# Kernel tuning notes

Hardware: AMD Instinct MI355X
Metric: run time of the kernel (lower is better)

Reference implementation:

```python
import jax, jax.numpy as jnp
import numpy as np

N, K, CIN, C, ET = 16, 128, 64, 64, 2  # batch, nodes, in-dim, hidden, edge types


def setup_inputs() -> dict:
    key = jax.random.key(0)
    ks = jax.random.split(key, 12)
    s = 0.05  # weight init scale
    return {
        "t": jnp.full((1,), 0.5, jnp.float32),
        "x": jax.random.normal(ks[0], (N, K, CIN), jnp.float32),
        "E": jax.random.uniform(ks[1], (N, K, K, ET), jnp.float32),
        # ConcatLinear: Linear(CIN+1 -> C) on cat([t, x])
        "W_lin": jax.random.normal(ks[2], (CIN + 1, C), jnp.float32) * s,
        "b_lin": jnp.zeros((C,), jnp.float32),
        # unary_passing: Linear(C,C) -> tanh -> Linear(C,C)
        "W_u1": jax.random.normal(ks[3], (C, C), jnp.float32) * s,
        "b_u1": jnp.zeros((C,), jnp.float32),
        "W_u2": jax.random.normal(ks[4], (C, C), jnp.float32) * s,
        "b_u2": jnp.zeros((C,), jnp.float32),
        # binary_passing[e]: Linear(2C,C) -> tanh -> Linear(C,C), stacked over edge types
        "W_b1": jax.random.normal(ks[5], (ET, 2 * C, C), jnp.float32) * s,
        "b_b1": jnp.zeros((ET, C), jnp.float32),
        "W_b2": jax.random.normal(ks[6], (ET, C, C), jnp.float32) * s,
        "b_b2": jnp.zeros((ET, C), jnp.float32),
    }


def reference(t, x, E, W_lin, b_lin, W_u1, b_u1, W_u2, b_u2, W_b1, b_b1, W_b2, b_b2):
    n, k, _ = x.shape
    # ConcatLinear: h = Linear(cat([t, x]))  -> [N, K, C]
    tt = jnp.broadcast_to(t.reshape(1, 1, 1).astype(x.dtype), (n, k, 1))
    h = jnp.concatenate([tt, x], axis=-1) @ W_lin + b_lin
    c = h.shape[-1]
    # unary message: MLP over nodes
    unary = jnp.tanh(h @ W_u1 + b_u1) @ W_u2 + b_u2  # [N, K, C]
    # all-pairs tensor: pair[n, i, j] = cat(h[n, j], h[n, i])  -> [N, K, K, 2C]
    pair = jnp.concatenate(
        [
            jnp.broadcast_to(h[:, None, :, :], (n, k, k, c)),
            jnp.broadcast_to(h[:, :, None, :], (n, k, k, c)),
        ],
        axis=-1,
    )
    # per-edge-type MLP (vectorized over edge types)
    hid = jnp.tanh(jnp.einsum('nijd,edh->enijh', pair, W_b1) + b_b1[:, None, None, None, :])
    msg = jnp.einsum('enijh,ehc->enijc', hid, W_b2) + b_b2[:, None, None, None, :]
    # weight by edge matrix and sum over edge types -> [N, K, K, C]
    msg = (msg * jnp.moveaxis(E, -1, 0)[..., None]).sum(axis=0)
    # reduce over sender dim (dim 1) and normalize by K
    binary = msg.sum(axis=1) / k  # [N, K, C]
    return unary + binary
```

## Files before the change

### kernel.cpp

```cpp
#include <hip/hip_runtime.h>

#define NB 16
#define KK 128
#define CC 64

__device__ __forceinline__ float tanh_from_e2x(float e2x) {
    return 1.f - 2.f * __builtin_amdgcn_rcpf(e2x + 1.f);
}

__global__ __launch_bounds__(256) void precompute_kernel(
    const float* __restrict__ t, const float* __restrict__ x,
    const float* __restrict__ W_lin, const float* __restrict__ b_lin,
    const float* __restrict__ W_u1, const float* __restrict__ b_u1,
    const float* __restrict__ W_u2, const float* __restrict__ b_u2,
    const float* __restrict__ W_b1, const float* __restrict__ b_b1,
    float* __restrict__ A2, float* __restrict__ B2, float* __restrict__ unary)
{
    const int tid  = threadIdx.x;
    const int lane = tid & 63;
    const int r    = blockIdx.x * 4 + (tid >> 6);

    const float xv = x[r * CC + lane];
    float h = fmaf(t[0], W_lin[lane], b_lin[lane]);
#pragma unroll 8
    for (int k = 0; k < CC; ++k) {
        float xk = __shfl(xv, k);
        h = fmaf(xk, W_lin[(k + 1) * CC + lane], h);
    }

    float u1 = b_u1[lane];
    float a0 = b_b1[lane], a1 = b_b1[CC + lane];
    float bb0 = 0.f, bb1 = 0.f;
#pragma unroll 4
    for (int k = 0; k < CC; ++k) {
        float hk = __shfl(h, k);
        u1  = fmaf(hk, W_u1[k * CC + lane], u1);
        a0  = fmaf(hk, W_b1[k * CC + lane], a0);
        bb0 = fmaf(hk, W_b1[(CC + k) * CC + lane], bb0);
        a1  = fmaf(hk, W_b1[2 * CC * CC + k * CC + lane], a1);
        bb1 = fmaf(hk, W_b1[2 * CC * CC + (CC + k) * CC + lane], bb1);
    }

    float tu = tanh_from_e2x(__expf(2.f * u1));
    float u2 = b_u2[lane];
#pragma unroll 8
    for (int k = 0; k < CC; ++k) {
        float uk = __shfl(tu, k);
        u2 = fmaf(uk, W_u2[k * CC + lane], u2);
    }

    const int idx = r * CC + lane;
    unary[idx] = u2;
    ((float2*)A2)[idx] = make_float2(2.f * a0, 2.f * a1);
    ((float2*)B2)[idx] = make_float2(2.f * bb0, 2.f * bb1);
}

__global__ __launch_bounds__(256) void binary_kernel(
    const float* __restrict__ E, const float* __restrict__ W_b2,
    const float* __restrict__ b_b2, const float* __restrict__ A2,
    const float* __restrict__ B2, const float* __restrict__ unary,
    float* __restrict__ out)
{
    __shared__ float Bs[KK * CC * 2];
    __shared__ float Es[4 * KK * 2];
    __shared__ float Gs[4 * CC * 2];

    const int tid = threadIdx.x;
    const int bid = blockIdx.x;
    const int n   = bid >> 5;
    const int j0  = (bid & 31) * 4;

    const float4* Bsrc = (const float4*)(B2 + n * KK * CC * 2);
    float4* Bdst = (float4*)Bs;
#pragma unroll
    for (int it = 0; it < 16; ++it) Bdst[tid + it * 256] = Bsrc[tid + it * 256];

    const float2* E2 = (const float2*)E;
    float2* Es2 = (float2*)Es;
#pragma unroll
    for (int it = 0; it < 2; ++it) {
        int v = tid + it * 256;
        int wv = v >> 7, i = v & 127;
        Es2[wv * KK + i] = E2[(n * KK + i) * KK + (j0 + wv)];
    }
    __syncthreads();

    const int lane = tid & 63;
    const int w    = tid >> 6;
    const int r    = n * KK + j0 + w;

    const float2 a2 = ((const float2*)A2)[r * CC + lane];
    const float2* BsRow = (const float2*)Bs;
    const float2* EsW   = ((const float2*)Es) + w * KK;

    float G0 = 0.f, G1 = 0.f;
#pragma unroll 8
    for (int i = 0; i < KK; ++i) {
        float2 bb = BsRow[i * CC + lane];
        float2 wg = EsW[i];
        float t0 = tanh_from_e2x(__expf(a2.x + bb.x));
        float t1 = tanh_from_e2x(__expf(a2.y + bb.y));
        G0 = fmaf(wg.x, t0, G0);
        G1 = fmaf(wg.y, t1, G1);
    }
    ((float2*)Gs)[w * CC + lane] = make_float2(G0, G1);

    float2 sv0 = EsW[lane], sv1 = EsW[CC + lane];
    float S0 = sv0.x + sv1.x, S1 = sv0.y + sv1.y;
#pragma unroll
    for (int m = 32; m; m >>= 1) {
        S0 += __shfl_xor(S0, m);
        S1 += __shfl_xor(S1, m);
    }
    __syncthreads();

    float acc = 0.f;
    const float2* GsW = ((const float2*)Gs) + w * CC;
#pragma unroll 8
    for (int hh = 0; hh < CC; ++hh) {
        float2 g = GsW[hh];
        acc = fmaf(g.x, W_b2[hh * CC + lane], acc);
        acc = fmaf(g.y, W_b2[CC * CC + hh * CC + lane], acc);
    }
    acc += b_b2[lane] * S0 + b_b2[CC + lane] * S1;

    out[r * CC + lane] = unary[r * CC + lane] + acc * (1.f / 128.f);
}

extern "C" void kernel_launch(void* const* d_in, const int* in_sizes, int n_in,
                              void* d_out, int out_size, void* d_ws, size_t ws_size,
                              hipStream_t stream) {
    const float* t     = (const float*)d_in[0];
    const float* x     = (const float*)d_in[1];
    const float* E     = (const float*)d_in[2];
    const float* W_lin = (const float*)d_in[3];
    const float* b_lin = (const float*)d_in[4];
    const float* W_u1  = (const float*)d_in[5];
    const float* b_u1  = (const float*)d_in[6];
    const float* W_u2  = (const float*)d_in[7];
    const float* b_u2  = (const float*)d_in[8];
    const float* W_b1  = (const float*)d_in[9];
    const float* b_b1  = (const float*)d_in[10];
    const float* W_b2  = (const float*)d_in[11];
    const float* b_b2  = (const float*)d_in[12];
    float* out = (float*)d_out;

    float* ws    = (float*)d_ws;
    float* A2    = ws;
    float* B2    = ws + 2 * NB * KK * CC;
    float* unary = ws + 4 * NB * KK * CC;

    precompute_kernel<<<NB * KK / 4, 256, 0, stream>>>(
        t, x, W_lin, b_lin, W_u1, b_u1, W_u2, b_u2, W_b1, b_b1, A2, B2, unary);
    binary_kernel<<<NB * (KK / 4), 256, 0, stream>>>(
        E, W_b2, b_b2, A2, B2, unary, out);
}
```

Measured before the change: 29.13 us.

## Split binary reduction across waves per receiver and stage W_b1 in LDS

The binary kernel now assigns one block per receiver node, with each of four waves handling 32 senders directly from global memory. Partial sums are reduced through shared memory, and the W_b2 projection is split across waves. This replaces the old per-block staging of the full 64KB B2 tile in LDS, aiming for many more blocks and no large LDS copy. The cost is extra syncs and less reuse of B2 across receivers. The precompute kernel stages W_b1 in 64KB of LDS with 512-thread blocks, and tanh now uses exp2 with a folded log2e scale.

Result: slower. 34.52 us (+18.5%).

```diff
diff --git a/kernel.cpp b/kernel.cpp
--- a/kernel.cpp
+++ b/kernel.cpp
@@ -4,11 +4,9 @@
 #define KK 128
 #define CC 64
 
-__device__ __forceinline__ float tanh_from_e2x(float e2x) {
-    return 1.f - 2.f * __builtin_amdgcn_rcpf(e2x + 1.f);
-}
+#define TSCALE 2.8853900817779268f
 
-__global__ __launch_bounds__(256) void precompute_kernel(
+__global__ __launch_bounds__(512) void precompute_kernel(
     const float* __restrict__ t, const float* __restrict__ x,
     const float* __restrict__ W_lin, const float* __restrict__ b_lin,
     const float* __restrict__ W_u1, const float* __restrict__ b_u1,
@@ -16,9 +14,19 @@
     const float* __restrict__ W_b1, const float* __restrict__ b_b1,
     float* __restrict__ A2, float* __restrict__ B2, float* __restrict__ unary)
 {
-    const int tid  = threadIdx.x;
+    __shared__ float Wb1s[2 * 2 * CC * CC];
+
+    const int tid = threadIdx.x;
+    {
+        const float4* src = (const float4*)W_b1;
+        float4* dst = (float4*)Wb1s;
+#pragma unroll
+        for (int it = 0; it < 8; ++it) dst[tid + it * 512] = src[tid + it * 512];
+    }
+    __syncthreads();
+
     const int lane = tid & 63;
-    const int r    = blockIdx.x * 4 + (tid >> 6);
+    const int r    = blockIdx.x * 8 + (tid >> 6);
 
     const float xv = x[r * CC + lane];
     float h = fmaf(t[0], W_lin[lane], b_lin[lane]);
@@ -35,13 +43,13 @@
     for (int k = 0; k < CC; ++k) {
         float hk = __shfl(h, k);
         u1  = fmaf(hk, W_u1[k * CC + lane], u1);
-        a0  = fmaf(hk, W_b1[k * CC + lane], a0);
-        bb0 = fmaf(hk, W_b1[(CC + k) * CC + lane], bb0);
-        a1  = fmaf(hk, W_b1[2 * CC * CC + k * CC + lane], a1);
-        bb1 = fmaf(hk, W_b1[2 * CC * CC + (CC + k) * CC + lane], bb1);
+        a0  = fmaf(hk, Wb1s[k * CC + lane], a0);
+        bb0 = fmaf(hk, Wb1s[(CC + k) * CC + lane], bb0);
+        a1  = fmaf(hk, Wb1s[2 * CC * CC + k * CC + lane], a1);
+        bb1 = fmaf(hk, Wb1s[2 * CC * CC + (CC + k) * CC + lane], bb1);
     }
 
-    float tu = tanh_from_e2x(__expf(2.f * u1));
+    float tu = fmaf(-2.f, __builtin_amdgcn_rcpf(__builtin_amdgcn_exp2f(TSCALE * u1) + 1.f), 1.f);
     float u2 = b_u2[lane];
 #pragma unroll 8
     for (int k = 0; k < CC; ++k) {
@@ -51,8 +59,8 @@
 
     const int idx = r * CC + lane;
     unary[idx] = u2;
-    ((float2*)A2)[idx] = make_float2(2.f * a0, 2.f * a1);
-    ((float2*)B2)[idx] = make_float2(2.f * bb0, 2.f * bb1);
+    ((float2*)A2)[idx] = make_float2(TSCALE * a0, TSCALE * a1);
+    ((float2*)B2)[idx] = make_float2(TSCALE * bb0, TSCALE * bb1);
 }
 
 __global__ __launch_bounds__(256) void binary_kernel(
@@ -61,70 +69,65 @@
     const float* __restrict__ B2, const float* __restrict__ unary,
     float* __restrict__ out)
 {
-    __shared__ float Bs[KK * CC * 2];
-    __shared__ float Es[4 * KK * 2];
     __shared__ float Gs[4 * CC * 2];
+    __shared__ float Ss[4 * 2];
+    __shared__ float Gred[CC * 2];
+    __shared__ float Accs[4 * CC];
 
-    const int tid = threadIdx.x;
-    const int bid = blockIdx.x;
-    const int n   = bid >> 5;
-    const int j0  = (bid & 31) * 4;
+    const int tid  = threadIdx.x;
+    const int lane = tid & 63;
+    const int w    = tid >> 6;
+    const int b    = blockIdx.x;
+    const int n    = b >> 7;
+    const int j    = b & 127;
+    const int rj   = n * KK + j;
 
-    const float4* Bsrc = (const float4*)(B2 + n * KK * CC * 2);
-    float4* Bdst = (float4*)Bs;
-#pragma unroll
-    for (int it = 0; it < 16; ++it) Bdst[tid + it * 256] = Bsrc[tid + it * 256];
+    const float2 a2 = ((const float2*)A2)[rj * CC + lane];
+    const float2* B2p = ((const float2*)B2) + (n * KK + w * 32) * CC + lane;
+    const float2* Ep  = ((const float2*)E)  + (n * KK + w * 32) * KK + j;
 
-    const float2* E2 = (const float2*)E;
-    float2* Es2 = (float2*)Es;
-#pragma unroll
-    for (int it = 0; it < 2; ++it) {
-        int v = tid + it * 256;
-        int wv = v >> 7, i = v & 127;
-        Es2[wv * KK + i] = E2[(n * KK + i) * KK + (j0 + wv)];
+    float G0 = 0.f, G1 = 0.f, S0 = 0.f, S1 = 0.f;
+#pragma unroll 8
+    for (int i = 0; i < 32; ++i) {
+        float2 bb = B2p[i * CC];
+        float2 wg = Ep[i * KK];
+        float e0 = __builtin_amdgcn_exp2f(a2.x + bb.x);
+        float e1 = __builtin_amdgcn_exp2f(a2.y + bb.y);
+        float t0 = fmaf(-2.f, __builtin_amdgcn_rcpf(e0 + 1.f), 1.f);
+        float t1 = fmaf(-2.f, __builtin_amdgcn_rcpf(e1 + 1.f), 1.f);
+        G0 = fmaf(wg.x, t0, G0);
+        G1 = fmaf(wg.y, t1, G1);
+        S0 += wg.x;
+        S1 += wg.y;
     }
+    ((float2*)Gs)[w * CC + lane] = make_float2(G0, G1);
+    if (lane == 0) ((float2*)Ss)[w] = make_float2(S0, S1);
     __syncthreads();
 
-    const int lane = tid & 63;
-    const int w    = tid >> 6;
-    const int r    = n * KK + j0 + w;
-
-    const float2 a2 = ((const float2*)A2)[r * CC + lane];
-    const float2* BsRow = (const float2*)Bs;
-    const float2* EsW   = ((const float2*)Es) + w * KK;
-
-    float G0 = 0.f, G1 = 0.f;
-#pragma unroll 8
-    for (int i = 0; i < KK; ++i) {
-        float2 bb = BsRow[i * CC + lane];
-        float2 wg = EsW[i];
-        float t0 = tanh_from_e2x(__expf(a2.x + bb.x));
-        float t1 = tanh_from_e2x(__expf(a2.y + bb.y));
-        G0 = fmaf(wg.x, t0, G0);
-        G1 = fmaf(wg.y, t1, G1);
-    }
-    ((float2*)Gs)[w * CC + lane] = make_float2(G0, G1);
-
-    float2 sv0 = EsW[lane], sv1 = EsW[CC + lane];
-    float S0 = sv0.x + sv1.x, S1 = sv0.y + sv1.y;
-#pragma unroll
-    for (int m = 32; m; m >>= 1) {
-        S0 += __shfl_xor(S0, m);
-        S1 += __shfl_xor(S1, m);
-    }
+    if (tid < 128) Gred[tid] = Gs[tid] + Gs[128 + tid] + Gs[256 + tid] + Gs[384 + tid];
     __syncthreads();
 
+    const float2 s0 = ((const float2*)Ss)[0], s1 = ((const float2*)Ss)[1];
+    const float2 s2 = ((const float2*)Ss)[2], s3 = ((const float2*)Ss)[3];
+    const float St0 = s0.x + s1.x + s2.x + s3.x;
+    const float St1 = s0.y + s1.y + s2.y + s3.y;
+
     float acc = 0.f;
-    const float2* GsW = ((const float2*)Gs) + w * CC;
-#pragma unroll 8
-    for (int hh = 0; hh < CC; ++hh) {
-        float2 g = GsW[hh];
+#pragma unroll
+    for (int hi = 0; hi < 16; ++hi) {
+        const int hh = w * 16 + hi;
+        float2 g = ((const float2*)Gred)[hh];
         acc = fmaf(g.x, W_b2[hh * CC + lane], acc);
         acc = fmaf(g.y, W_b2[CC * CC + hh * CC + lane], acc);
     }
-    acc += b_b2[lane] * S0 + b_b2[CC + lane] * S1;
+    Accs[w * CC + lane] = acc;
+    __syncthreads();
 
-    out[r * CC + lane] = unary[r * CC + lane] + acc * (1.f / 128.f);
+    if (w == 0) {
+        float a = Accs[lane] + Accs[CC + lane] + Accs[2 * CC + lane] + Accs[3 * CC + lane];
+        a += b_b2[lane] * St0 + b_b2[CC + lane] * St1;
+        out[rj * CC + lane] = unary[rj * CC + lane] + a * (1.f / 128.f);
+    }
 }
 
 extern "C" void kernel_launch(void* const* d_in, const int* in_sizes, int n_in,
@@ -150,8 +153,8 @@
     float* B2    = ws + 2 * NB * KK * CC;
     float* unary = ws + 4 * NB * KK * CC;
 
-    precompute_kernel<<<NB * KK / 4, 256, 0, stream>>>(
+    precompute_kernel<<<NB * KK / 8, 512, 0, stream>>>(
         t, x, W_lin, b_lin, W_u1, b_u1, W_u2, b_u2, W_b1, b_b1, A2, B2, unary);
-    binary_kernel<<<NB * (KK / 4), 256, 0, stream>>>(
+    binary_kernel<<<NB * KK, 256, 0, stream>>>(
         E, W_b2, b_b2, A2, B2, unary, out);
 }
```
